# Kernel optimization log

Measured on AMD Instinct MI355X. Metric: run time of the kernel, lower is better.

## Reference

```python
import jax, jax.numpy as jnp
import numpy as np

N = 4_000_000
EPS = 1e-6

# Quaternion layout: (w, x, y, z)

def _qmul(q1, q2):
    w1, v1 = q1[..., :1], q1[..., 1:]
    w2, v2 = q2[..., :1], q2[..., 1:]
    w = w1 * w2 - jnp.sum(v1 * v2, axis=-1, keepdims=True)
    v = w1 * v2 + w2 * v1 + jnp.cross(v1, v2)
    return jnp.concatenate([w, v], axis=-1)

def _qinv(q):
    # unit quaternion inverse = conjugate
    return q * jnp.array([1.0, -1.0, -1.0, -1.0], dtype=q.dtype)

def _qlog(q):
    # SO(3) log map: returns tangent vector theta * axis, shape [..., 3]
    w, v = q[..., 0], q[..., 1:]
    nv = jnp.linalg.norm(v, axis=-1)
    small = nv < EPS
    nv_safe = jnp.where(small, 1.0, nv)
    theta = 2.0 * jnp.arctan2(nv, w)
    # small-angle limit: theta/nv -> 2/w
    scale = jnp.where(small, 2.0 / w, theta / nv_safe)
    return v * scale[..., None]

def setup_inputs() -> dict:
    key = jax.random.key(0)
    k1, k2 = jax.random.split(key)
    a = jax.random.normal(k1, (N, 4), dtype=jnp.float32)
    a = a / jnp.linalg.norm(a, axis=-1, keepdims=True)
    idd = jax.random.normal(k2, (N, 4), dtype=jnp.float32)
    idd = idd / jnp.linalg.norm(idd, axis=-1, keepdims=True)
    return {"a": a, "idd": idd}

def reference(a, idd):
    # (a.Inv() @ idd).Log().norm()
    rel = _qmul(_qinv(a), idd)          # [N,4] relative rotation
    tangent = _qlog(rel)                 # [N,3] log map
    return jnp.linalg.norm(tangent)      # scalar Frobenius norm
```

## Files before the change

### kernel.cpp

```cpp
#include <hip/hip_runtime.h>
#include <math.h>

#define BLOCK 256
#define UNROLL 12
#define WTILE (64 * UNROLL)

__device__ __forceinline__ float theta_sq(float4 qa, float4 qb) {
    float w1 = qa.x, x1 = -qa.y, y1 = -qa.z, z1 = -qa.w;
    float w2 = qb.x, x2 = qb.y,  y2 = qb.z,  z2 = qb.w;
    float w  = w1*w2 - (x1*x2 + y1*y2 + z1*z2);
    float vx = w1*x2 + w2*x1 + (y1*z2 - z1*y2);
    float vy = w1*y2 + w2*y1 + (z1*x2 - x1*z2);
    float vz = w1*z2 + w2*z1 + (x1*y2 - y1*x2);
    float nv2 = vx*vx + vy*vy + vz*vz;
    float nv  = sqrtf(nv2);
    if (nv < 1e-6f) {
        float s = 2.0f / w;
        return nv2 * s * s;
    }
    float rn = rsqrtf(w*w + nv2);
    float c  = w * rn;
    float ac = fabsf(c);
    float p  = ((-0.0187293f*ac + 0.0742610f)*ac - 0.2121144f)*ac + 1.5707288f;
    float r  = sqrtf(fmaxf(1.0f - ac, 0.0f)) * p;
    float acosc = (c >= 0.0f) ? r : (3.14159265358979f - r);
    float theta = 2.0f * acosc;
    return theta * theta;
}

__global__ __launch_bounds__(BLOCK) void geo_loss_kernel(
        const float4* __restrict__ a,
        const float4* __restrict__ idd,
        float* __restrict__ partials, int n) {
    const int tid  = threadIdx.x;
    const int lane = tid & 63;
    const int gw   = (blockIdx.x * BLOCK + tid) >> 6;
    const int wbase = gw * WTILE;
    float acc = 0.0f;

    if (wbase + WTILE <= n) {
        float4 qa[UNROLL], qb[UNROLL];
        #pragma unroll
        for (int k = 0; k < UNROLL; k++) qa[k] = a[wbase + k * 64 + lane];
        #pragma unroll
        for (int k = 0; k < UNROLL; k++) qb[k] = idd[wbase + k * 64 + lane];
        #pragma unroll
        for (int k = 0; k < UNROLL; k++) acc += theta_sq(qa[k], qb[k]);
    } else if (wbase < n) {
        for (int k = 0; k < UNROLL; k++) {
            int idx = wbase + k * 64 + lane;
            if (idx < n) acc += theta_sq(a[idx], idd[idx]);
        }
    }

    #pragma unroll
    for (int off = 32; off > 0; off >>= 1)
        acc += __shfl_down(acc, off, 64);
    __shared__ float smem[BLOCK / 64];
    int wid = tid >> 6;
    if (lane == 0) smem[wid] = acc;
    __syncthreads();
    if (tid == 0)
        partials[blockIdx.x] = smem[0] + smem[1] + smem[2] + smem[3];
}

__global__ __launch_bounds__(BLOCK) void finalize_kernel(
        const float* __restrict__ partials,
        float* __restrict__ out, int nparts) {
    float acc = 0.0f;
    for (int i = threadIdx.x; i < nparts; i += BLOCK)
        acc += partials[i];
    #pragma unroll
    for (int off = 32; off > 0; off >>= 1)
        acc += __shfl_down(acc, off, 64);
    __shared__ float smem[BLOCK / 64];
    int lane = threadIdx.x & 63;
    int wid  = threadIdx.x >> 6;
    if (lane == 0) smem[wid] = acc;
    __syncthreads();
    if (threadIdx.x == 0)
        out[0] = sqrtf(smem[0] + smem[1] + smem[2] + smem[3]);
}

extern "C" void kernel_launch(void* const* d_in, const int* in_sizes, int n_in,
                              void* d_out, int out_size, void* d_ws, size_t ws_size,
                              hipStream_t stream) {
    const float4* a   = (const float4*)d_in[0];
    const float4* idd = (const float4*)d_in[1];
    int n = in_sizes[0] / 4;
    float* ws = (float*)d_ws;

    int nwaves = (n + WTILE - 1) / WTILE;
    int grid   = (nwaves + (BLOCK / 64) - 1) / (BLOCK / 64);
    geo_loss_kernel<<<grid, BLOCK, 0, stream>>>(a, idd, ws, n);
    finalize_kernel<<<1, BLOCK, 0, stream>>>(ws, (float*)d_out, grid);
}
```

Measured before the change: 144.6 us.

## Stage quaternion loads through LDS with direct global-to-LDS loads in persistent grid

Replaces per-thread register loads with global_load_lds transfers into shared memory, processed by a fixed 1024-block grid that grid-strides over 256-element stages per wave. A scalar tail loop handles leftover elements. The intent is to bypass register staging and use a persistent launch. In exchange, each wave now has fewer loads in flight per wait and fully serialises load and compute, with no double buffering.

```diff
diff --git a/kernel.cpp b/kernel.cpp
--- a/kernel.cpp
+++ b/kernel.cpp
@@ -2,8 +2,9 @@
 #include <math.h>
 
 #define BLOCK 256
-#define UNROLL 12
-#define WTILE (64 * UNROLL)
+#define GRID  1024
+#define NW    (GRID * (BLOCK/64))
+#define SELEM 256
 
 __device__ __forceinline__ float theta_sq(float4 qa, float4 qb) {
     float w1 = qa.x, x1 = -qa.y, y1 = -qa.z, z1 = -qa.w;
@@ -32,32 +33,45 @@
         const float4* __restrict__ a,
         const float4* __restrict__ idd,
         float* __restrict__ partials, int n) {
+    __shared__ float4 sA[4][SELEM];
+    __shared__ float4 sB[4][SELEM];
     const int tid  = threadIdx.x;
     const int lane = tid & 63;
-    const int gw   = (blockIdx.x * BLOCK + tid) >> 6;
-    const int wbase = gw * WTILE;
+    const int wid  = tid >> 6;
+    const int gwave = blockIdx.x * (BLOCK / 64) + wid;
+    const int nstages = n / SELEM;
     float acc = 0.0f;
 
-    if (wbase + WTILE <= n) {
-        float4 qa[UNROLL], qb[UNROLL];
+    for (int s = gwave; s < nstages; s += NW) {
+        const int ebase = s * SELEM;
         #pragma unroll
-        for (int k = 0; k < UNROLL; k++) qa[k] = a[wbase + k * 64 + lane];
+        for (int k = 0; k < 4; k++) {
+            __builtin_amdgcn_global_load_lds(
+                (const __attribute__((address_space(1))) void*)(a + ebase + k * 64 + lane),
+                (__attribute__((address_space(3))) void*)(&sA[wid][k * 64]),
+                16, 0, 0);
+        }
         #pragma unroll
-        for (int k = 0; k < UNROLL; k++) qb[k] = idd[wbase + k * 64 + lane];
+        for (int k = 0; k < 4; k++) {
+            __builtin_amdgcn_global_load_lds(
+                (const __attribute__((address_space(1))) void*)(idd + ebase + k * 64 + lane),
+                (__attribute__((address_space(3))) void*)(&sB[wid][k * 64]),
+                16, 0, 0);
+        }
+        __builtin_amdgcn_s_waitcnt(0x0F70);
         #pragma unroll
-        for (int k = 0; k < UNROLL; k++) acc += theta_sq(qa[k], qb[k]);
-    } else if (wbase < n) {
-        for (int k = 0; k < UNROLL; k++) {
-            int idx = wbase + k * 64 + lane;
-            if (idx < n) acc += theta_sq(a[idx], idd[idx]);
-        }
+        for (int j = 0; j < 4; j++)
+            acc += theta_sq(sA[wid][j * 64 + lane], sB[wid][j * 64 + lane]);
     }
+
+    for (int idx = nstages * SELEM + blockIdx.x * BLOCK + tid; idx < n;
+         idx += GRID * BLOCK)
+        acc += theta_sq(a[idx], idd[idx]);
 
     #pragma unroll
     for (int off = 32; off > 0; off >>= 1)
         acc += __shfl_down(acc, off, 64);
     __shared__ float smem[BLOCK / 64];
-    int wid = tid >> 6;
     if (lane == 0) smem[wid] = acc;
     __syncthreads();
     if (tid == 0)
@@ -90,8 +104,6 @@
     int n = in_sizes[0] / 4;
     float* ws = (float*)d_ws;
 
-    int nwaves = (n + WTILE - 1) / WTILE;
-    int grid   = (nwaves + (BLOCK / 64) - 1) / (BLOCK / 64);
-    geo_loss_kernel<<<grid, BLOCK, 0, stream>>>(a, idd, ws, n);
-    finalize_kernel<<<1, BLOCK, 0, stream>>>(ws, (float*)d_out, grid);
+    geo_loss_kernel<<<GRID, BLOCK, 0, stream>>>(a, idd, ws, n);
+    finalize_kernel<<<1, BLOCK, 0, stream>>>(ws, (float*)d_out, GRID);
 }
```

Result: no change. 143.3 us (-0.9%).
